# Kernel tuning notes

Hardware: AMD Instinct MI355X
Metric: run time of the kernel (lower is better)

The kernel has to match this reference:

```python
import jax, jax.numpy as jnp
import numpy as np

K = 7      # number of neighbor volumes (init k)
PS = 7     # patch size (unfold.ps / wpsum.ps)
WS = 13    # search window side -> O = WS*WS candidates per query
WR = WS // 2
EPS = 1e-6


def setup_inputs() -> dict:
    key = jax.random.key(0)
    k1, k2, k3, k4 = jax.random.split(key, 4)
    C, E, H, W = 64, 32, 128, 128
    return {
        "x": jax.random.normal(k1, (C, H, W), jnp.float32),
        "xe": jax.random.normal(k2, (E, H, W), jnp.float32),
        "ye": jax.random.normal(k3, (E, H, W), jnp.float32),
        "log_temp": 0.1 * jax.random.normal(k4, (1, H, W), jnp.float32),
    }


def _box_sum(img, ps):
    # img: [B, H, W] -> centered ps x ps box sum with zero padding, same shape
    kern = jnp.ones((1, 1, ps, ps), img.dtype)
    return jax.lax.conv_general_dilated(img[:, None], kern, (1, 1), "SAME")[:, 0]


def _forward(x, xe, ye, log_temp):
    C, H, W_ = x.shape
    E = xe.shape[0]
    offs = np.stack(np.meshgrid(np.arange(WS), np.arange(WS), indexing="ij"), -1).reshape(-1, 2)
    O = offs.shape[0]
    dis = jnp.asarray(offs[:, 0]); djs = jnp.asarray(offs[:, 1])

    xe_pad = jnp.pad(xe, ((0, 0), (WR, WR), (WR, WR)))
    x_pad = jnp.pad(x, ((0, 0), (WR, WR), (WR, WR)))

    # ---- search: per-candidate patch SSD between query/database embeddings ----
    def per_off_dist(di, dj):
        xs = jax.lax.dynamic_slice(xe_pad, (0, di, dj), (E, H, W_))
        return jnp.sum((ye - xs) ** 2, axis=0)  # [H, W] pixel-wise sq dist

    diff2 = jax.vmap(per_off_dist)(dis, djs)        # [O, H, W]
    dists = -_box_sum(diff2, PS)                    # patch SSD, negated

    # ---- temperature: avgpool of log_temp over the ps x ps patch (avgpool=True) ----
    lt = _box_sum(log_temp, PS) / float(PS * PS)    # [1, H, W]
    temp = jnp.exp(lt)                              # temp_bias=1 -> log bias 0

    # ---- NeuralNearestNeighbors: k rounds of temp-softmax with exclusion ----
    logits = dists / temp                           # [O, H, W]
    Ws = []
    for _ in range(K):  # small structural loop over k neighbor volumes
        w = jax.nn.softmax(logits, axis=0)
        Ws.append(w)
        logits = logits + jnp.log(jnp.clip(1.0 - w, EPS))
    Wk = jnp.stack(Ws, 0)                           # [K, O, H, W]

    # ---- wpsum + fold fused: for stride-1 centered patches the patch offset
    # cancels, so out[k,c,y] = sum_o boxsum_ps(W[k,o])[y] * x[c, y + off(o)] ----
    Wsum = _box_sum(Wk.reshape(K * O, H, W_), PS).reshape(K, O, H, W_)
    Wsum_o = jnp.moveaxis(Wsum, 1, 0)               # [O, K, H, W]

    def body(out, inp):
        di, dj, wso = inp
        xs = jax.lax.dynamic_slice(x_pad, (0, di, dj), (C, H, W_))
        return out + wso[:, None] * xs[None], None  # [K, C, H, W]

    out0 = jnp.zeros((K, C, H, W_), x.dtype)
    out, _ = jax.lax.scan(body, out0, (dis, djs, Wsum_o))
    return out.reshape(K * C, H, W_)


def reference(x, xe, ye, log_temp):
    return _forward(x, xe, ye, log_temp)
```

## Files before the change

### kernel.cpp

```cpp
#include <hip/hip_runtime.h>
#include <hip/hip_bf16.h>
#include <hip/hip_fp16.h>

#define HW 16384

using u16 = unsigned short;
using u32 = unsigned int;
typedef __attribute__((ext_vector_type(2))) float f32x2;

__device__ __forceinline__ u16 f2h(float f) {
    __half h = __float2half(f);
    return __builtin_bit_cast(u16, h);
}
__device__ __forceinline__ void dot2acc(float& acc, u32 a, u32 b) {
    asm("v_dot2_f32_f16 %0, %1, %2, %0" : "+v"(acc) : "v"(a), "v"(b));
}
#define SELLO 0x05040100u
#define SELHI 0x07060302u

__global__ __launch_bounds__(256) void k_prep(
        const float* __restrict__ x, const float* __restrict__ xe,
        const float* __restrict__ ye,
        u16* __restrict__ xh, float* __restrict__ xeT,
        float* __restrict__ yeT, float* __restrict__ nx, float* __restrict__ ny) {
    int y = blockIdx.x * 256 + threadIdx.x;

#pragma unroll
    for (int c = 0; c < 64; c++)
        xh[c * HW + y] = f2h(x[c * HW + y]);

    float sx = 0.f, sy = 0.f;
#pragma unroll
    for (int e0 = 0; e0 < 32; e0 += 4) {
        float4 v = make_float4(xe[(e0 + 0) * HW + y], xe[(e0 + 1) * HW + y],
                               xe[(e0 + 2) * HW + y], xe[(e0 + 3) * HW + y]);
        *reinterpret_cast<float4*>(xeT + y * 32 + e0) = v;
        sx += v.x * v.x + v.y * v.y + v.z * v.z + v.w * v.w;
        float4 u = make_float4(ye[(e0 + 0) * HW + y], ye[(e0 + 1) * HW + y],
                               ye[(e0 + 2) * HW + y], ye[(e0 + 3) * HW + y]);
        *reinterpret_cast<float4*>(yeT + y * 32 + e0) = u;
        sy += u.x * u.x + u.y * u.y + u.z * u.z + u.w * u.w;
    }
    nx[y] = sx;
    ny[y] = sy;
}

__global__ __launch_bounds__(256) void k_norms(
        const float* __restrict__ ny, const float* __restrict__ lt,
        float2* __restrict__ st) {
    int y = blockIdx.x * 256 + threadIdx.x;
    int py = y >> 7, px = y & 127;
    float s = 0.f, t = 0.f;
    for (int dy = -3; dy <= 3; dy++)
        for (int dx = -3; dx <= 3; dx++) {
            int yy = py + dy, xx = px + dx;
            if ((unsigned)yy < 128u && (unsigned)xx < 128u) {
                int p = yy * 128 + xx;
                s += ny[p];
                t += lt[p];
            }
        }
    float tinv = __expf(-t * (1.0f / 49.0f));
    st[y] = make_float2(tinv, tinv * s);
}

__global__ __launch_bounds__(1024) void k_logits(
        const float* __restrict__ xeT, const float* __restrict__ yeT,
        const float* __restrict__ nxg, const float2* __restrict__ st,
        float* __restrict__ logits) {
#pragma clang fp contract(fast)
    __shared__ __align__(16) char arena[123904];
    float* s_xe = (float*)arena;
    float* s_nx = (float*)(arena + 95744);
    float* s_d2 = (float*)(arena + 98736);
    float* s_hs = (float*)arena;

    int di = blockIdx.x;
    int tile = blockIdx.y;
    int h0 = (tile >> 3) * 16, w0 = (tile & 7) * 16;
    int gr0 = h0 + di - 9, gc0 = w0 - 9;
    int tid = threadIdx.x;

    for (int idx = tid; idx < 748 * 8; idx += 1024) {
        int cell = idx >> 3, q = idx & 7;
        int r = cell / 34, c = cell - r * 34;
        int gy = gr0 + r, gx = gc0 + c;
        float4 v = make_float4(0.f, 0.f, 0.f, 0.f);
        if ((unsigned)gy < 128u && (unsigned)gx < 128u)
            v = *reinterpret_cast<const float4*>(xeT + (size_t)(gy * 128 + gx) * 32 + q * 4);
        *reinterpret_cast<float4*>(s_xe + cell * 32 + ((q ^ (cell & 7)) << 2)) = v;
    }
    for (int idx = tid; idx < 748; idx += 1024) {
        int r = idx / 34, c = idx - r * 34;
        int gy = gr0 + r, gx = gc0 + c;
        float v = 0.f;
        if ((unsigned)gy < 128u && (unsigned)gx < 128u) v = nxg[gy * 128 + gx];
        s_nx[idx] = v;
    }
    __syncthreads();

    if (tid < 484) {
        int zr = tid / 22, zc = tid - zr * 22;
        int gy = h0 - 3 + zr, gx = w0 - 3 + zc;
        bool zin = ((unsigned)gy < 128u) && ((unsigned)gx < 128u);
        f32x2 yv[16];
#pragma unroll
        for (int j = 0; j < 16; j++) yv[j] = (f32x2){0.f, 0.f};
        if (zin) {
            const float* yp = yeT + (size_t)(gy * 128 + gx) * 32;
#pragma unroll
            for (int j = 0; j < 8; j++) {
                float4 t = *reinterpret_cast<const float4*>(yp + j * 4);
                yv[2 * j] = (f32x2){t.x, t.y};
                yv[2 * j + 1] = (f32x2){t.z, t.w};
            }
        }
        int cell0 = zr * 34 + zc;
#pragma unroll
        for (int dj = 0; dj < 13; dj++) {
            int cell = cell0 + dj;
            const float* bp = s_xe + cell * 32;
            int sw = cell & 7;
            f32x2 a0 = {0.f, 0.f}, a1 = {0.f, 0.f};
#pragma unroll
            for (int q = 0; q < 8; q++) {
                float4 xv = *reinterpret_cast<const float4*>(bp + ((q ^ sw) << 2));
                a0 += ((f32x2){xv.x, xv.y}) * yv[2 * q];
                a1 += ((f32x2){xv.z, xv.w}) * yv[2 * q + 1];
            }
            float cr = a0.x + a0.y + a1.x + a1.y;
            float d2v = fmaf(-2.f, cr, s_nx[cell]);
            s_d2[dj * 484 + tid] = zin ? d2v : 0.f;
        }
    }
    __syncthreads();

    for (int idx = tid; idx < 4576; idx += 1024) {
        int dj = idx / 352, rem = idx - dj * 352;
        int r = rem >> 4, c = rem & 15;
        const float* p = s_d2 + dj * 484 + r * 22 + c;
        float s = p[0] + p[1] + p[2] + p[3] + p[4] + p[5] + p[6];
        s_hs[(dj * 22 + r) * 16 + c] = s;
    }
    __syncthreads();

    for (int idx = tid; idx < 3328; idx += 1024) {
        int dj = idx >> 8, rem = idx & 255;
        int i = rem >> 4, jj = rem & 15;
        const float* p = s_hs + (dj * 22 + i) * 16 + jj;
        float s = p[0] + p[16] + p[32] + p[48] + p[64] + p[80] + p[96];
        int y = (h0 + i) * 128 + (w0 + jj);
        float2 ab = st[y];
        logits[(di * 13 + dj) * HW + y] = -fmaf(ab.x, s, ab.y);
    }
}

__global__ __launch_bounds__(256) void k_softmax(
        const float* __restrict__ logits, u16* __restrict__ Wkt) {
    __shared__ float s_lg[169 * 34];
    int tid = threadIdx.x;
    int y0 = blockIdx.x * 32;
    for (int idx = tid; idx < 169 * 32; idx += 256) {
        int o = idx >> 5, p = idx & 31;
        s_lg[o * 34 + p] = logits[o * HW + y0 + p];
    }
    __syncthreads();
    int pix = tid >> 3, t = tid & 7;
    int y = y0 + pix;
    float l[22];
#pragma unroll
    for (int j = 0; j < 22; j++) {
        int o = t + 8 * j;
        l[j] = (o < 169) ? s_lg[o * 34 + pix] : -3e38f;
    }
    u32 wp0[22], wp1[22], wp2[22], wp3[22];
#pragma unroll
    for (int j = 0; j < 22; j++) { wp0[j] = 0u; wp1[j] = 0u; wp2[j] = 0u; wp3[j] = 0u; }

    float e[22];
#pragma unroll
    for (int k = 0; k < 7; k++) {
        float m = -3e38f;
#pragma unroll
        for (int j = 0; j < 22; j++) m = fmaxf(m, l[j]);
        m = fmaxf(m, __shfl_xor(m, 1));
        m = fmaxf(m, __shfl_xor(m, 2));
        m = fmaxf(m, __shfl_xor(m, 4));
        float s = 0.f;
#pragma unroll
        for (int j = 0; j < 22; j++) { e[j] = __expf(l[j] - m); s += e[j]; }
        s += __shfl_xor(s, 1);
        s += __shfl_xor(s, 2);
        s += __shfl_xor(s, 4);
        float rs = 1.0f / s;
#pragma unroll
        for (int j = 0; j < 22; j++) {
            float w = e[j] * rs;
            u32 h = (u32)f2h(w);
            if (k == 0) wp0[j] |= h;
            else if (k == 1) wp0[j] |= h << 16;
            else if (k == 2) wp1[j] |= h;
            else if (k == 3) wp1[j] |= h << 16;
            else if (k == 4) wp2[j] |= h;
            else if (k == 5) wp2[j] |= h << 16;
            else wp3[j] |= h;
            if (k < 6) l[j] += __logf(fmaxf(1.0f - w, 1e-6f));
        }
    }
#pragma unroll
    for (int j = 0; j < 22; j++) {
        int o = t + 8 * j;
        if (o < 169)
            *reinterpret_cast<uint4*>(Wkt + (o * HW + y) * 8) =
                make_uint4(wp0[j], wp1[j], wp2[j], wp3[j]);
    }
}

__global__ __launch_bounds__(256) void k_wsum(
        const u16* __restrict__ Wkt, u32* __restrict__ WsP) {
    __shared__ u16 s_w[38 * 39 * 8];
    __shared__ u16 s_v[32 * 38 * 8];
    int o2 = blockIdx.x;
    int di = o2 / 7, djp = o2 - di * 7;
    int oA = di * 13 + 2 * djp;
    bool hasB = (djp < 6);
    int tile = blockIdx.y;
    int h0 = (tile >> 2) * 32, w0 = (tile & 3) * 32;
    int tid = threadIdx.x;

    auto stage = [&](int o) {
        const u16* src = Wkt + (size_t)o * (HW * 8);
        for (int idx = tid; idx < 38 * 38; idx += 256) {
            int r = idx / 38, c = idx - r * 38;
            int gy = h0 - 3 + r, gx = w0 - 3 + c;
            uint4 v = make_uint4(0u, 0u, 0u, 0u);
            if ((unsigned)gy < 128u && (unsigned)gx < 128u)
                v = *reinterpret_cast<const uint4*>(src + (gy * 128 + gx) * 8);
            *reinterpret_cast<uint4*>(s_w + (r * 39 + c) * 8) = v;
        }
    };
    auto vert = [&]() {
        for (int u = tid; u < 1216; u += 256) {
            int r = u / 38, c = u - r * 38;
            __half2 s0 = __builtin_bit_cast(__half2, 0u);
            __half2 s1 = s0, s2 = s0, s3 = s0;
#pragma unroll
            for (int d = 0; d < 7; d++) {
                uint4 q = *reinterpret_cast<const uint4*>(s_w + ((r + d) * 39 + c) * 8);
                s0 = __hadd2(s0, __builtin_bit_cast(__half2, q.x));
                s1 = __hadd2(s1, __builtin_bit_cast(__half2, q.y));
                s2 = __hadd2(s2, __builtin_bit_cast(__half2, q.z));
                s3 = __hadd2(s3, __builtin_bit_cast(__half2, q.w));
            }
            *reinterpret_cast<uint4*>(s_v + (r * 38 + c) * 8) = make_uint4(
                __builtin_bit_cast(u32, s0), __builtin_bit_cast(u32, s1),
                __builtin_bit_cast(u32, s2), __builtin_bit_cast(u32, s3));
        }
    };
    auto horiz = [&](uint4 (&rr)[4]) {
#pragma unroll
        for (int i = 0; i < 4; i++) {
            int u = tid + i * 256;
            int r = u >> 5, cx = u & 31;
            __half2 s0 = __builtin_bit_cast(__half2, 0u);
            __half2 s1 = s0, s2 = s0, s3 = s0;
#pragma unroll
            for (int d = 0; d < 7; d++) {
                uint4 q = *reinterpret_cast<const uint4*>(s_v + (r * 38 + cx + d) * 8);
                s0 = __hadd2(s0, __builtin_bit_cast(__half2, q.x));
                s1 = __hadd2(s1, __builtin_bit_cast(__half2, q.y));
                s2 = __hadd2(s2, __builtin_bit_cast(__half2, q.z));
                s3 = __hadd2(s3, __builtin_bit_cast(__half2, q.w));
            }
            rr[i] = make_uint4(
                __builtin_bit_cast(u32, s0), __builtin_bit_cast(u32, s1),
                __builtin_bit_cast(u32, s2), __builtin_bit_cast(u32, s3));
        }
    };

    uint4 rA[4], rB[4];
#pragma unroll
    for (int i = 0; i < 4; i++) rB[i] = make_uint4(0u, 0u, 0u, 0u);

    stage(oA);
    __syncthreads();
    vert();
    __syncthreads();
    horiz(rA);
    if (hasB) {
        __syncthreads();
        stage(oA + 1);
        __syncthreads();
        vert();
        __syncthreads();
        horiz(rB);
    }

#pragma unroll
    for (int i = 0; i < 4; i++) {
        int u = tid + i * 256;
        int r = u >> 5, cx = u & 31;
        int y = (h0 + r) * 128 + (w0 + cx);
        u32* dst = WsP + ((size_t)o2 * HW + y) * 8;
        uint4 lo = make_uint4(
            __builtin_amdgcn_perm(rB[i].x, rA[i].x, SELLO),
            __builtin_amdgcn_perm(rB[i].x, rA[i].x, SELHI),
            __builtin_amdgcn_perm(rB[i].y, rA[i].y, SELLO),
            __builtin_amdgcn_perm(rB[i].y, rA[i].y, SELHI));
        uint4 hi = make_uint4(
            __builtin_amdgcn_perm(rB[i].z, rA[i].z, SELLO),
            __builtin_amdgcn_perm(rB[i].z, rA[i].z, SELHI),
            __builtin_amdgcn_perm(rB[i].w, rA[i].w, SELLO),
            0u);
        *reinterpret_cast<uint4*>(dst) = lo;
        *reinterpret_cast<uint4*>(dst + 4) = hi;
    }
}

__global__ __launch_bounds__(256, 3) void k_agg(
        const u16* __restrict__ xh, const u32* __restrict__ WsP,
        float* __restrict__ out) {
    __shared__ u16 s_x[16 * 16 * 32];
    int tb = blockIdx.x & 255;
    int csplit = blockIdx.x >> 8;
    int h0 = (tb >> 3) * 4, w0 = (tb & 7) * 16;
    int tid = threadIdx.x;

    for (int it = tid; it < 1024; it += 256) {
        int ch = it >> 6;
        int r = (it >> 2) & 15;
        int c0 = (it & 3) * 8;
        int gy = h0 - 6 + r, gx0 = w0 - 6 + c0;
        int gc = csplit * 16 + ch;
        uint4 v = make_uint4(0u, 0u, 0u, 0u);
        if ((unsigned)gy < 128u) {
            const u16* src = xh + (size_t)gc * HW + gy * 128;
            if (gx0 >= 0 && gx0 <= 120) {
                v = *reinterpret_cast<const uint4*>(src + gx0);
            } else {
                auto pk = [&](int gx) -> u32 {
                    u32 lo = ((unsigned)gx < 128u) ? (u32)src[gx] : 0u;
                    u32 hi = ((unsigned)(gx + 1) < 128u) ? (u32)src[gx + 1] : 0u;
                    return lo | (hi << 16);
                };
                v = make_uint4(pk(gx0), pk(gx0 + 2), pk(gx0 + 4), pk(gx0 + 6));
            }
        }
        *reinterpret_cast<uint4*>(s_x + (ch * 16 + r) * 32 + c0) = v;
    }
    __syncthreads();

    int cc = tid >> 6, pix = tid & 63;
    int pr = pix >> 4, pc = pix & 15;
    int y = (h0 + pr) * 128 + (w0 + pc);
    const u32* wsrc = WsP + (size_t)y * 8;
    const u32* s_x32 = reinterpret_cast<const u32*>(s_x);
    u32 sh = (u32)(pc & 1) * 16;
    int cbase_dw = (pc >> 1);

    float acc[7][4];
#pragma unroll
    for (int k = 0; k < 7; k++)
#pragma unroll
        for (int q = 0; q < 4; q++) acc[k][q] = 0.f;

    auto loadW = [&](int di, uint4 (&A)[7], uint4 (&B)[7]) {
        const u32* wdi = wsrc + (size_t)(di * 7) * (HW * 8);
#pragma unroll
        for (int djp = 0; djp < 7; djp++) {
            const u32* wp = wdi + (size_t)djp * (HW * 8);
            A[djp] = *reinterpret_cast<const uint4*>(wp);
            B[djp] = *reinterpret_cast<const uint4*>(wp + 4);
        }
    };
    auto compute = [&](int di, const uint4 (&A)[7], const uint4 (&B)[7]) {
        int rowb = (pr + di) * 16 + cbase_dw;
#pragma unroll
        for (int djp = 0; djp < 7; djp++) {
#pragma unroll
            for (int q = 0; q < 4; q++) {
                const u32* p = s_x32 + ((cc * 4 + q) * 256 + rowb + djp);
                u32 d0 = p[0], d1 = p[1];
                u32 x2 = __builtin_amdgcn_alignbit(d1, d0, sh);
                dot2acc(acc[0][q], A[djp].x, x2);
                dot2acc(acc[1][q], A[djp].y, x2);
                dot2acc(acc[2][q], A[djp].z, x2);
                dot2acc(acc[3][q], A[djp].w, x2);
                dot2acc(acc[4][q], B[djp].x, x2);
                dot2acc(acc[5][q], B[djp].y, x2);
                dot2acc(acc[6][q], B[djp].z, x2);
            }
        }
    };

    uint4 WA[7], WB[7], WC[7], WD[7];
    loadW(0, WA, WB);
#pragma unroll 1
    for (int di = 0; di < 12; di += 2) {
        loadW(di + 1, WC, WD);
        compute(di, WA, WB);
        loadW(di + 2, WA, WB);
        compute(di + 1, WC, WD);
    }
    compute(12, WA, WB);

    int cb = csplit * 16 + cc * 4;
#pragma unroll
    for (int k = 0; k < 7; k++)
#pragma unroll
        for (int q = 0; q < 4; q++)
            out[(k * 64 + cb + q) * HW + y] = acc[k][q];
}

extern "C" void kernel_launch(void* const* d_in, const int* in_sizes, int n_in,
                              void* d_out, int out_size, void* d_ws, size_t ws_size,
                              hipStream_t stream) {
    (void)in_sizes; (void)n_in; (void)out_size; (void)ws_size;
    const float* x  = (const float*)d_in[0];
    const float* xe = (const float*)d_in[1];
    const float* ye = (const float*)d_in[2];
    const float* lt = (const float*)d_in[3];
    float* out = (float*)d_out;
    char* ws = (char*)d_ws;

    u16*   xh     = (u16*)(ws + 0);
    float* xeT    = (float*)(ws + 2097152u);
    float* yeT    = (float*)(ws + 4194304u);
    u16*   Wkt    = (u16*)(ws + 6291456u);
    float* logits = (float*)(ws + 50593792u);
    u32*   WsP    = (u32*)(ws + 50593792u);
    float*  nx = (float*)(ws + 6291456u);
    float*  ny = (float*)(ws + 6291456u + 65536u);
    float2* st = (float2*)(ws + 6291456u + 131072u);

    k_prep<<<64, 256, 0, stream>>>(x, xe, ye, xh, xeT, yeT, nx, ny);
    k_norms<<<64, 256, 0, stream>>>(ny, lt, st);
    k_logits<<<dim3(13, 64), 1024, 0, stream>>>(xeT, yeT, nx, st, logits);
    k_softmax<<<512, 256, 0, stream>>>(logits, Wkt);
    k_wsum<<<dim3(91, 16), 256, 0, stream>>>(Wkt, WsP);
    k_agg<<<1024, 256, 0, stream>>>(xh, WsP, out);
}
```

Baseline: 157.0 us.

## Process all 64 channels per agg block and reuse LDS row loads across offsets

The aggregation kernel now has each 512-thread block handle all 64 channels of a tile instead of splitting channels across four blocks. Each thread accumulates 8 channels rather than 4, so every weight vector loaded from global memory is reused twice as much. The 7 horizontal-offset LDS reads are replaced by 8 consecutive dword loads per row, shared across all offsets. The trade-off is more registers (56 accumulators), 64KB of LDS per block, and only 256 blocks, which lowers occupancy and grid parallelism.

```diff
diff --git a/kernel.cpp b/kernel.cpp
--- a/kernel.cpp
+++ b/kernel.cpp
@@ -317,24 +317,24 @@
     }
 }
 
-__global__ __launch_bounds__(256, 3) void k_agg(
+__global__ __launch_bounds__(512, 2) void k_agg(
         const u16* __restrict__ xh, const u32* __restrict__ WsP,
         float* __restrict__ out) {
-    __shared__ u16 s_x[16 * 16 * 32];
-    int tb = blockIdx.x & 255;
-    int csplit = blockIdx.x >> 8;
+    __shared__ u16 s_x[64 * 16 * 32];
+    int tb = blockIdx.x;
     int h0 = (tb >> 3) * 4, w0 = (tb & 7) * 16;
     int tid = threadIdx.x;
 
-    for (int it = tid; it < 1024; it += 256) {
+#pragma unroll
+    for (int i = 0; i < 8; i++) {
+        int it = tid + i * 512;
         int ch = it >> 6;
         int r = (it >> 2) & 15;
         int c0 = (it & 3) * 8;
         int gy = h0 - 6 + r, gx0 = w0 - 6 + c0;
-        int gc = csplit * 16 + ch;
         uint4 v = make_uint4(0u, 0u, 0u, 0u);
         if ((unsigned)gy < 128u) {
-            const u16* src = xh + (size_t)gc * HW + gy * 128;
+            const u16* src = xh + (size_t)ch * HW + gy * 128;
             if (gx0 >= 0 && gx0 <= 120) {
                 v = *reinterpret_cast<const uint4*>(src + gx0);
             } else {
@@ -356,13 +356,13 @@
     const u32* wsrc = WsP + (size_t)y * 8;
     const u32* s_x32 = reinterpret_cast<const u32*>(s_x);
     u32 sh = (u32)(pc & 1) * 16;
-    int cbase_dw = (pc >> 1);
-
-    float acc[7][4];
+    int base0 = cc * 8 * 256 + (pc >> 1);
+
+    float acc[7][8];
 #pragma unroll
     for (int k = 0; k < 7; k++)
 #pragma unroll
-        for (int q = 0; q < 4; q++) acc[k][q] = 0.f;
+        for (int q = 0; q < 8; q++) acc[k][q] = 0.f;
 
     auto loadW = [&](int di, uint4 (&A)[7], uint4 (&B)[7]) {
         const u32* wdi = wsrc + (size_t)(di * 7) * (HW * 8);
@@ -374,22 +374,48 @@
         }
     };
     auto compute = [&](int di, const uint4 (&A)[7], const uint4 (&B)[7]) {
-        int rowb = (pr + di) * 16 + cbase_dw;
-#pragma unroll
-        for (int djp = 0; djp < 7; djp++) {
-#pragma unroll
-            for (int q = 0; q < 4; q++) {
-                const u32* p = s_x32 + ((cc * 4 + q) * 256 + rowb + djp);
-                u32 d0 = p[0], d1 = p[1];
-                u32 x2 = __builtin_amdgcn_alignbit(d1, d0, sh);
-                dot2acc(acc[0][q], A[djp].x, x2);
-                dot2acc(acc[1][q], A[djp].y, x2);
-                dot2acc(acc[2][q], A[djp].z, x2);
-                dot2acc(acc[3][q], A[djp].w, x2);
-                dot2acc(acc[4][q], B[djp].x, x2);
-                dot2acc(acc[5][q], B[djp].y, x2);
-                dot2acc(acc[6][q], B[djp].z, x2);
-            }
+        int rowoff = (pr + di) * 16;
+#pragma unroll
+        for (int q = 0; q < 8; q++) {
+            const u32* p = s_x32 + base0 + q * 256 + rowoff;
+            u32 f0 = p[0], f1 = p[1], f2 = p[2], f3 = p[3];
+            u32 f4 = p[4], f5 = p[5], f6 = p[6], f7 = p[7];
+            u32 x2;
+            x2 = __builtin_amdgcn_alignbit(f1, f0, sh);
+            dot2acc(acc[0][q], A[0].x, x2); dot2acc(acc[1][q], A[0].y, x2);
+            dot2acc(acc[2][q], A[0].z, x2); dot2acc(acc[3][q], A[0].w, x2);
+            dot2acc(acc[4][q], B[0].x, x2); dot2acc(acc[5][q], B[0].y, x2);
+            dot2acc(acc[6][q], B[0].z, x2);
+            x2 = __builtin_amdgcn_alignbit(f2, f1, sh);
+            dot2acc(acc[0][q], A[1].x, x2); dot2acc(acc[1][q], A[1].y, x2);
+            dot2acc(acc[2][q], A[1].z, x2); dot2acc(acc[3][q], A[1].w, x2);
+            dot2acc(acc[4][q], B[1].x, x2); dot2acc(acc[5][q], B[1].y, x2);
+            dot2acc(acc[6][q], B[1].z, x2);
+            x2 = __builtin_amdgcn_alignbit(f3, f2, sh);
+            dot2acc(acc[0][q], A[2].x, x2); dot2acc(acc[1][q], A[2].y, x2);
+            dot2acc(acc[2][q], A[2].z, x2); dot2acc(acc[3][q], A[2].w, x2);
+            dot2acc(acc[4][q], B[2].x, x2); dot2acc(acc[5][q], B[2].y, x2);
+            dot2acc(acc[6][q], B[2].z, x2);
+            x2 = __builtin_amdgcn_alignbit(f4, f3, sh);
+            dot2acc(acc[0][q], A[3].x, x2); dot2acc(acc[1][q], A[3].y, x2);
+            dot2acc(acc[2][q], A[3].z, x2); dot2acc(acc[3][q], A[3].w, x2);
+            dot2acc(acc[4][q], B[3].x, x2); dot2acc(acc[5][q], B[3].y, x2);
+            dot2acc(acc[6][q], B[3].z, x2);
+            x2 = __builtin_amdgcn_alignbit(f5, f4, sh);
+            dot2acc(acc[0][q], A[4].x, x2); dot2acc(acc[1][q], A[4].y, x2);
+            dot2acc(acc[2][q], A[4].z, x2); dot2acc(acc[3][q], A[4].w, x2);
+            dot2acc(acc[4][q], B[4].x, x2); dot2acc(acc[5][q], B[4].y, x2);
+            dot2acc(acc[6][q], B[4].z, x2);
+            x2 = __builtin_amdgcn_alignbit(f6, f5, sh);
+            dot2acc(acc[0][q], A[5].x, x2); dot2acc(acc[1][q], A[5].y, x2);
+            dot2acc(acc[2][q], A[5].z, x2); dot2acc(acc[3][q], A[5].w, x2);
+            dot2acc(acc[4][q], B[5].x, x2); dot2acc(acc[5][q], B[5].y, x2);
+            dot2acc(acc[6][q], B[5].z, x2);
+            x2 = __builtin_amdgcn_alignbit(f7, f6, sh);
+            dot2acc(acc[0][q], A[6].x, x2); dot2acc(acc[1][q], A[6].y, x2);
+            dot2acc(acc[2][q], A[6].z, x2); dot2acc(acc[3][q], A[6].w, x2);
+            dot2acc(acc[4][q], B[6].x, x2); dot2acc(acc[5][q], B[6].y, x2);
+            dot2acc(acc[6][q], B[6].z, x2);
         }
     };
 
@@ -404,12 +430,11 @@
     }
     compute(12, WA, WB);
 
-    int cb = csplit * 16 + cc * 4;
 #pragma unroll
     for (int k = 0; k < 7; k++)
 #pragma unroll
-        for (int q = 0; q < 4; q++)
-            out[(k * 64 + cb + q) * HW + y] = acc[k][q];
+        for (int q = 0; q < 8; q++)
+            out[(k * 64 + cc * 8 + q) * HW + y] = acc[k][q];
 }
 
 extern "C" void kernel_launch(void* const* d_in, const int* in_sizes, int n_in,
@@ -438,5 +463,5 @@
     k_logits<<<dim3(13, 64), 1024, 0, stream>>>(xeT, yeT, nx, st, logits);
     k_softmax<<<512, 256, 0, stream>>>(logits, Wkt);
     k_wsum<<<dim3(91, 16), 256, 0, stream>>>(Wkt, WsP);
-    k_agg<<<1024, 256, 0, stream>>>(xh, WsP, out);
-}
+    k_agg<<<256, 512, 0, stream>>>(xh, WsP, out);
+}
```

Result: no change. 155.2 us (-1.1%).

## Restructure aggregation blocks to cover all channels and reuse weight loads

Applied to the files above, without the earlier changes.

The aggregation kernel now uses 512-thread blocks that each cover a 2x16 pixel tile across all 64 channels, instead of 256-thread blocks over a 4x16 tile and 16 channels split four ways. Each weight vector loaded from global memory is therefore reused across more channels per block, and total weight traffic drops because the channel split is gone. The inner loop also preloads 8 shared-memory dwords per channel row into registers and double-buffers them against the dot-product work, replacing two LDS reads per tap. This costs a larger shared tile with more halo rows per output row, and higher register pressure that may limit occupancy.

```diff
diff --git a/kernel.cpp b/kernel.cpp
--- a/kernel.cpp
+++ b/kernel.cpp
@@ -317,24 +317,23 @@
     }
 }
 
-__global__ __launch_bounds__(256, 3) void k_agg(
+__global__ __launch_bounds__(512, 2) void k_agg(
         const u16* __restrict__ xh, const u32* __restrict__ WsP,
         float* __restrict__ out) {
-    __shared__ u16 s_x[16 * 16 * 32];
-    int tb = blockIdx.x & 255;
-    int csplit = blockIdx.x >> 8;
-    int h0 = (tb >> 3) * 4, w0 = (tb & 7) * 16;
+    __shared__ u16 s_x[64 * 456];
+    int tb = blockIdx.x;
+    int h0 = (tb >> 3) * 2, w0 = (tb & 7) * 16;
     int tid = threadIdx.x;
 
-    for (int it = tid; it < 1024; it += 256) {
-        int ch = it >> 6;
-        int r = (it >> 2) & 15;
-        int c0 = (it & 3) * 8;
-        int gy = h0 - 6 + r, gx0 = w0 - 6 + c0;
-        int gc = csplit * 16 + ch;
+#pragma unroll
+    for (int i = 0; i < 7; i++) {
+        int it = tid + i * 512;
+        int ch = it / 56, rem = it - ch * 56;
+        int r = rem >> 2, j = rem & 3;
+        int gy = h0 - 6 + r, gx0 = w0 - 6 + 8 * j;
         uint4 v = make_uint4(0u, 0u, 0u, 0u);
         if ((unsigned)gy < 128u) {
-            const u16* src = xh + (size_t)gc * HW + gy * 128;
+            const u16* src = xh + (size_t)ch * HW + gy * 128;
             if (gx0 >= 0 && gx0 <= 120) {
                 v = *reinterpret_cast<const uint4*>(src + gx0);
             } else {
@@ -346,17 +345,17 @@
                 v = make_uint4(pk(gx0), pk(gx0 + 2), pk(gx0 + 4), pk(gx0 + 6));
             }
         }
-        *reinterpret_cast<uint4*>(s_x + (ch * 16 + r) * 32 + c0) = v;
-    }
-    __syncthreads();
-
-    int cc = tid >> 6, pix = tid & 63;
+        *reinterpret_cast<uint4*>(s_x + ch * 456 + r * 32 + 8 * j) = v;
+    }
+    __syncthreads();
+
+    int cc = tid >> 5, pix = tid & 31;
     int pr = pix >> 4, pc = pix & 15;
     int y = (h0 + pr) * 128 + (w0 + pc);
     const u32* wsrc = WsP + (size_t)y * 8;
     const u32* s_x32 = reinterpret_cast<const u32*>(s_x);
     u32 sh = (u32)(pc & 1) * 16;
-    int cbase_dw = (pc >> 1);
+    int base0 = cc * 912 + (pc >> 1);
 
     float acc[7][4];
 #pragma unroll
@@ -373,43 +372,56 @@
             B[djp] = *reinterpret_cast<const uint4*>(wp + 4);
         }
     };
-    auto compute = [&](int di, const uint4 (&A)[7], const uint4 (&B)[7]) {
-        int rowb = (pr + di) * 16 + cbase_dw;
+    auto loadX = [&](u32 (&buf)[8], int dwoff) {
+        const u32* p = s_x32 + dwoff;
+#pragma unroll
+        for (int j = 0; j < 8; j++) buf[j] = p[j];
+    };
+    auto computeQ = [&](const u32 (&f)[8], const uint4 (&A)[7],
+                        const uint4 (&B)[7], int q) {
 #pragma unroll
         for (int djp = 0; djp < 7; djp++) {
-#pragma unroll
-            for (int q = 0; q < 4; q++) {
-                const u32* p = s_x32 + ((cc * 4 + q) * 256 + rowb + djp);
-                u32 d0 = p[0], d1 = p[1];
-                u32 x2 = __builtin_amdgcn_alignbit(d1, d0, sh);
-                dot2acc(acc[0][q], A[djp].x, x2);
-                dot2acc(acc[1][q], A[djp].y, x2);
-                dot2acc(acc[2][q], A[djp].z, x2);
-                dot2acc(acc[3][q], A[djp].w, x2);
-                dot2acc(acc[4][q], B[djp].x, x2);
-                dot2acc(acc[5][q], B[djp].y, x2);
-                dot2acc(acc[6][q], B[djp].z, x2);
-            }
-        }
+            u32 x2 = __builtin_amdgcn_alignbit(f[djp + 1], f[djp], sh);
+            dot2acc(acc[0][q], A[djp].x, x2);
+            dot2acc(acc[1][q], A[djp].y, x2);
+            dot2acc(acc[2][q], A[djp].z, x2);
+            dot2acc(acc[3][q], A[djp].w, x2);
+            dot2acc(acc[4][q], B[djp].x, x2);
+            dot2acc(acc[5][q], B[djp].y, x2);
+            dot2acc(acc[6][q], B[djp].z, x2);
+        }
+    };
+    auto computeDi = [&](int di, int nextdi, const uint4 (&A)[7],
+                         const uint4 (&B)[7], u32 (&xb)[8], u32 (&xt)[8]) {
+        int ro = base0 + (pr + di) * 16;
+        loadX(xt, ro + 228);
+        computeQ(xb, A, B, 0);
+        loadX(xb, ro + 2 * 228);
+        computeQ(xt, A, B, 1);
+        loadX(xt, ro + 3 * 228);
+        computeQ(xb, A, B, 2);
+        loadX(xb, base0 + (pr + nextdi) * 16);
+        computeQ(xt, A, B, 3);
     };
 
     uint4 WA[7], WB[7], WC[7], WD[7];
+    u32 xb[8], xt[8];
     loadW(0, WA, WB);
+    loadX(xb, base0 + pr * 16);
 #pragma unroll 1
     for (int di = 0; di < 12; di += 2) {
         loadW(di + 1, WC, WD);
-        compute(di, WA, WB);
+        computeDi(di, di + 1, WA, WB, xb, xt);
         loadW(di + 2, WA, WB);
-        compute(di + 1, WC, WD);
-    }
-    compute(12, WA, WB);
-
-    int cb = csplit * 16 + cc * 4;
+        computeDi(di + 1, di + 2, WC, WD, xb, xt);
+    }
+    computeDi(12, 12, WA, WB, xb, xt);
+
 #pragma unroll
     for (int k = 0; k < 7; k++)
 #pragma unroll
         for (int q = 0; q < 4; q++)
-            out[(k * 64 + cb + q) * HW + y] = acc[k][q];
+            out[(k * 64 + cc * 4 + q) * HW + y] = acc[k][q];
 }
 
 extern "C" void kernel_launch(void* const* d_in, const int* in_sizes, int n_in,
@@ -438,5 +450,5 @@
     k_logits<<<dim3(13, 64), 1024, 0, stream>>>(xeT, yeT, nx, st, logits);
     k_softmax<<<512, 256, 0, stream>>>(logits, Wkt);
     k_wsum<<<dim3(91, 16), 256, 0, stream>>>(Wkt, WsP);
-    k_agg<<<1024, 256, 0, stream>>>(xh, WsP, out);
-}
+    k_agg<<<512, 512, 0, stream>>>(xh, WsP, out);
+}
```

After: 162.5 us. 3.5% more time.
